# Optimization experiments

Measured on AMD Instinct MI355X. Metric: run time of the kernel, lower is better.

The kernel has to match this reference:

```python
import jax, jax.numpy as jnp
import numpy as np

D_MODEL = 1024; N_HEAD = 16; HD = 64
D_STATE = 128; D_CONV = 4; EXPAND = 2; HEADDIM = 64
D_INNER = EXPAND * D_MODEL          # 2048
NHEADS = D_INNER // HEADDIM         # 32
FFN = 4 * D_MODEL                   # 4096
B, T = 2, 1024


def rmsnorm(x, eps=1e-6):
    # FastSimpleRMSNorm: no learnable weight
    return x * jax.lax.rsqrt(jnp.mean(x * x, axis=-1, keepdims=True) + eps)


def causal_dwconv(x, w, b):
    # x: (..., T, C), w: (C, K), b: (C,). Causal depthwise conv (left pad K-1).
    K = w.shape[1]
    t = x.shape[-2]
    pad = [(0, 0)] * (x.ndim - 2) + [(K - 1, 0), (0, 0)]
    xp = jnp.pad(x, pad)
    y = jnp.zeros_like(x) + b
    for k in range(K):
        y = y + w[:, k] * jax.lax.slice_in_dim(xp, k, k + t, axis=-2)
    return y


def block_forward(x, W_in, conv_w, conv_b, A_log, Dm, dt_bias, mnorm_w, W_out,
                  W_qkv, W_cproj, qconv_w, qconv_b, kconv_w, kconv_b, vconv_w, vconv_b,
                  time_maa_k, time_maa_r, W_key, W_rec, W_val):
    Bsz, Tn, _ = x.shape
    # ---- Mamba2 branch ----
    h = rmsnorm(x)
    zxbcdt = h @ W_in                                  # (B,T,2*D_INNER+2*N+H)
    z = zxbcdt[..., :D_INNER]
    xBC = zxbcdt[..., D_INNER:2 * D_INNER + 2 * D_STATE]
    dt = zxbcdt[..., -NHEADS:]
    xBC = jax.nn.silu(causal_dwconv(xBC, conv_w, conv_b))
    xm = xBC[..., :D_INNER]
    Bm = xBC[..., D_INNER:D_INNER + D_STATE]           # (B,T,N)
    Cm = xBC[..., -D_STATE:]                           # (B,T,N)
    dt = jax.nn.softplus(dt + dt_bias)                 # (B,T,H)
    A = -jnp.exp(A_log)                                # (H,)
    xh = xm.reshape(Bsz, Tn, NHEADS, HEADDIM)          # (B,T,H,P)

    def step(hstate, inp):
        dt_t, x_t, B_t, C_t = inp                      # (B,H),(B,H,P),(B,N),(B,N)
        dA = jnp.exp(dt_t * A)                         # (B,H)
        hstate = hstate * dA[..., None, None] + (dt_t[..., None] * x_t)[..., None] * B_t[:, None, None, :]
        y_t = jnp.einsum('bhpn,bn->bhp', hstate, C_t)
        return hstate, y_t

    h0 = jnp.zeros((Bsz, NHEADS, HEADDIM, D_STATE), x.dtype)
    _, ys = jax.lax.scan(step, h0, (jnp.swapaxes(dt, 0, 1), jnp.swapaxes(xh, 0, 1),
                                    jnp.swapaxes(Bm, 0, 1), jnp.swapaxes(Cm, 0, 1)))
    y = jnp.swapaxes(ys, 0, 1) + xh * Dm[:, None]      # (B,T,H,P)
    y = y.reshape(Bsz, Tn, D_INNER) * jax.nn.silu(z)   # gated
    y = y * jax.lax.rsqrt(jnp.mean(y * y, axis=-1, keepdims=True) + 1e-5) * mnorm_w
    x = x + y @ W_out

    # ---- MQA with depthwise convs ----
    h = rmsnorm(x)
    qkv = h @ W_qkv                                    # (B,T,D_MODEL+2*HD)
    q = qkv[..., :D_MODEL].reshape(Bsz, Tn, N_HEAD, HD).transpose(0, 2, 1, 3)  # (B,H,T,D)
    k = qkv[..., D_MODEL:D_MODEL + HD]                 # (B,T,D) single kv head
    v = qkv[..., -HD:]
    q = causal_dwconv(q, qconv_w, qconv_b)
    k = causal_dwconv(k, kconv_w, kconv_b)
    v = causal_dwconv(v, vconv_w, vconv_b)
    scores = jnp.einsum('bhtd,bsd->bhts', q, k) / np.float32(np.sqrt(HD))
    mask = jnp.tril(jnp.ones((Tn, Tn), bool))
    scores = jnp.where(mask, scores, -jnp.inf)
    p = jax.nn.softmax(scores, axis=-1)
    y = jnp.einsum('bhts,bsd->bhtd', p, v)
    y = y.transpose(0, 2, 1, 3).reshape(Bsz, Tn, D_MODEL)
    x = x + y @ W_cproj

    # ---- RWKV CMix FFN ----
    h = rmsnorm(x)
    xx = jnp.pad(h, ((0, 0), (1, 0), (0, 0)))[:, :Tn] - h   # time_shift(x) - x
    xk = h + xx * time_maa_k
    xr = h + xx * time_maa_r
    kf = jnp.square(jax.nn.relu(xk @ W_key))           # ReLU^2
    kv = kf @ W_val
    x = x + jax.nn.sigmoid(xr @ W_rec) * kv
    return x


def setup_inputs() -> dict:
    key = jax.random.key(0)
    ks = jax.random.split(key, 16)
    def w(k, shape, sc=0.02):
        return jax.random.normal(k, shape, jnp.float32) * sc
    x = jax.random.normal(ks[0], (B, T, D_MODEL), jnp.float32)
    W_in = w(ks[1], (D_MODEL, 2 * D_INNER + 2 * D_STATE + NHEADS))
    conv_w = w(ks[2], (D_INNER + 2 * D_STATE, D_CONV), 0.2)
    conv_b = jnp.zeros((D_INNER + 2 * D_STATE,), jnp.float32)
    A_log = jnp.log(jnp.arange(1, NHEADS + 1, dtype=jnp.float32))
    Dm = jnp.ones((NHEADS,), jnp.float32)
    dt_bias = w(ks[3], (NHEADS,), 0.5)
    mnorm_w = jnp.ones((D_INNER,), jnp.float32)
    W_out = w(ks[4], (D_INNER, D_MODEL))
    W_qkv = w(ks[5], (D_MODEL, D_MODEL + 2 * HD))
    W_cproj = w(ks[6], (D_MODEL, D_MODEL))
    qconv_w = w(ks[7], (HD, 3), 0.3); qconv_b = jnp.zeros((HD,), jnp.float32)
    kconv_w = w(ks[8], (HD, 3), 0.3); kconv_b = jnp.zeros((HD,), jnp.float32)
    vconv_w = w(ks[9], (HD, 3), 0.3); vconv_b = jnp.zeros((HD,), jnp.float32)
    ddd = jnp.arange(D_MODEL, dtype=jnp.float32) / D_MODEL
    time_maa_k = 1.0 - ddd  # layer_id=0 -> ratio_1_to_almost0 = 1
    time_maa_r = 1.0 - ddd
    W_key = w(ks[10], (D_MODEL, FFN))
    W_rec = w(ks[11], (D_MODEL, D_MODEL))
    W_val = w(ks[12], (FFN, D_MODEL))
    return dict(x=x, W_in=W_in, conv_w=conv_w, conv_b=conv_b, A_log=A_log, Dm=Dm,
                dt_bias=dt_bias, mnorm_w=mnorm_w, W_out=W_out, W_qkv=W_qkv, W_cproj=W_cproj,
                qconv_w=qconv_w, qconv_b=qconv_b, kconv_w=kconv_w, kconv_b=kconv_b,
                vconv_w=vconv_w, vconv_b=vconv_b, time_maa_k=time_maa_k, time_maa_r=time_maa_r,
                W_key=W_key, W_rec=W_rec, W_val=W_val)


def reference(x, W_in, conv_w, conv_b, A_log, Dm, dt_bias, mnorm_w, W_out,
              W_qkv, W_cproj, qconv_w, qconv_b, kconv_w, kconv_b, vconv_w, vconv_b,
              time_maa_k, time_maa_r, W_key, W_rec, W_val):
    return block_forward(x, W_in, conv_w, conv_b, A_log, Dm, dt_bias, mnorm_w, W_out,
                         W_qkv, W_cproj, qconv_w, qconv_b, kconv_w, kconv_b, vconv_w, vconv_b,
                         time_maa_k, time_maa_r, W_key, W_rec, W_val)
```

## Files before the change

kernel.cpp:

```cpp
#include <hip/hip_runtime.h>
#include <hip/hip_bf16.h>
#include <math.h>

#define BB 2
#define TT 1024
#define BT (BB*TT)
#define DM 1024
#define DI 2048
#define DS 128
#define NHS 32
#define PDIM 64
#define NHA 16
#define HD 64
#define FFN_ 4096
#define NZX 4384
#define NXBC 2304
#define NXBCD 2336
#define CL 128
#define NC 8

typedef __hip_bfloat16 bf16;
typedef short bf16x8 __attribute__((ext_vector_type(8)));
typedef float f32x4 __attribute__((ext_vector_type(4)));

__device__ __forceinline__ float b2f(bf16 v){ return __bfloat162float(v); }
__device__ __forceinline__ bf16 f2b(float v){ return __float2bfloat16(v); }

__global__ void k_rms_in(const float* __restrict__ xin, float* __restrict__ X,
                         bf16* __restrict__ H) {
  int row = blockIdx.x;
  int tid = threadIdx.x;
  const float* xr = xin + (size_t)row * DM;
  float v[4]; float ss = 0.f;
  #pragma unroll
  for (int i = 0; i < 4; ++i) { v[i] = xr[tid*4+i]; ss += v[i]*v[i]; }
  __shared__ float red[256];
  red[tid] = ss; __syncthreads();
  for (int s = 128; s > 0; s >>= 1) { if (tid < s) red[tid] += red[tid+s]; __syncthreads(); }
  float scale = rsqrtf(red[0]/(float)DM + 1e-6f);
  float* Xr = X + (size_t)row*DM; bf16* Hr = H + (size_t)row*DM;
  #pragma unroll
  for (int i = 0; i < 4; ++i) { Xr[tid*4+i] = v[i]; Hr[tid*4+i] = f2b(v[i]*scale); }
}

__global__ void k_rms_f32(const float* __restrict__ X, bf16* __restrict__ H) {
  int row = blockIdx.x;
  int tid = threadIdx.x;
  const float* xr = X + (size_t)row * DM;
  float v[4]; float ss = 0.f;
  #pragma unroll
  for (int i = 0; i < 4; ++i) { v[i] = xr[tid*4+i]; ss += v[i]*v[i]; }
  __shared__ float red[256];
  red[tid] = ss; __syncthreads();
  for (int s = 128; s > 0; s >>= 1) { if (tid < s) red[tid] += red[tid+s]; __syncthreads(); }
  float scale = rsqrtf(red[0]/(float)DM + 1e-6f);
  bf16* Hr = H + (size_t)row*DM;
  #pragma unroll
  for (int i = 0; i < 4; ++i) Hr[tid*4+i] = f2b(v[i]*scale);
}

__global__ void k_tcast(const float* __restrict__ W, bf16* __restrict__ Wt,
                        int K, int N) {
  __shared__ float t[32][33];
  int tx = threadIdx.x, ty = threadIdx.y;
  int n0 = blockIdx.x*32, k0 = blockIdx.y*32;
  #pragma unroll
  for (int i = 0; i < 4; ++i) {
    int k = k0 + ty + i*8, n = n0 + tx;
    t[ty + i*8][tx] = (n < N) ? W[(size_t)k*N + n] : 0.f;
  }
  __syncthreads();
  #pragma unroll
  for (int i = 0; i < 4; ++i) {
    int n = n0 + ty + i*8, k = k0 + tx;
    Wt[(size_t)n*K + k] = f2b(t[tx][ty + i*8]);
  }
}

template<int EPI, bool ADD, bool OUTBF>
__global__ __launch_bounds__(256)
void mfma_gemm(const bf16* __restrict__ A, const bf16* __restrict__ Bt,
               float* __restrict__ C, bf16* __restrict__ Cbf,
               int M, int N, int K) {
  __shared__ bf16 As[128*32];
  __shared__ bf16 Bs[128*32];
  int tid = threadIdx.x;
  int wave = tid >> 6, lane = tid & 63;
  int m_l = lane & 15, quad = lane >> 4;
  int wr = (wave & 1) * 64, wc = (wave >> 1) * 64;
  int row0 = blockIdx.y * 128, col0 = blockIdx.x * 128;
  f32x4 acc[4][4];
  #pragma unroll
  for (int i = 0; i < 4; ++i)
    #pragma unroll
    for (int j = 0; j < 4; ++j) acc[i][j] = (f32x4){0.f,0.f,0.f,0.f};
  int r_a = tid >> 2;
  int kc  = (tid & 3) * 8;
  for (int k0 = 0; k0 < K; k0 += 32) {
    uint4 av0 = *(const uint4*)&A [(size_t)(row0      + r_a) * K + k0 + kc];
    uint4 av1 = *(const uint4*)&A [(size_t)(row0 + 64 + r_a) * K + k0 + kc];
    uint4 bv0 = *(const uint4*)&Bt[(size_t)(col0      + r_a) * K + k0 + kc];
    uint4 bv1 = *(const uint4*)&Bt[(size_t)(col0 + 64 + r_a) * K + k0 + kc];
    __syncthreads();
    *(uint4*)&As[(     r_a) * 32 + kc] = av0;
    *(uint4*)&As[(64 + r_a) * 32 + kc] = av1;
    *(uint4*)&Bs[(     r_a) * 32 + kc] = bv0;
    *(uint4*)&Bs[(64 + r_a) * 32 + kc] = bv1;
    __syncthreads();
    bf16x8 af[4], bfv[4];
    #pragma unroll
    for (int i = 0; i < 4; ++i) af[i]  = *(const bf16x8*)&As[(wr + i*16 + m_l)*32 + quad*8];
    #pragma unroll
    for (int j = 0; j < 4; ++j) bfv[j] = *(const bf16x8*)&Bs[(wc + j*16 + m_l)*32 + quad*8];
    #pragma unroll
    for (int i = 0; i < 4; ++i)
      #pragma unroll
      for (int j = 0; j < 4; ++j)
        acc[i][j] = __builtin_amdgcn_mfma_f32_16x16x32_bf16(af[i], bfv[j], acc[i][j], 0, 0, 0);
  }
  #pragma unroll
  for (int i = 0; i < 4; ++i) {
    #pragma unroll
    for (int j = 0; j < 4; ++j) {
      int col = col0 + wc + j*16 + m_l;
      if (col < N) {
        #pragma unroll
        for (int r = 0; r < 4; ++r) {
          int row = row0 + wr + i*16 + quad*4 + r;
          float v = acc[i][j][r];
          if (EPI == 1) { v = fmaxf(v, 0.f); v = v*v; }
          else if (EPI == 2) v = 1.f/(1.f + __expf(-v));
          if (OUTBF)      Cbf[(size_t)row*N + col] = f2b(v);
          else if (ADD)   C[(size_t)row*N + col] += v;
          else            C[(size_t)row*N + col]  = v;
        }
      }
    }
  }
}

__global__ __launch_bounds__(256)
void mfma_sk32(const bf16* __restrict__ A, const bf16* __restrict__ Bt,
               float* __restrict__ P0, float* __restrict__ P1,
               float* __restrict__ P2, float* __restrict__ P3,
               int M, int N, int K, int kchunk) {
  __shared__ bf16 As[128*32];
  __shared__ bf16 Bs[128*32];
  int tid = threadIdx.x;
  int wave = tid >> 6, lane = tid & 63;
  int m_l = lane & 15, quad = lane >> 4;
  int wr = (wave & 1) * 64, wc = (wave >> 1) * 64;
  int row0 = blockIdx.y * 128, col0 = blockIdx.x * 128;
  int kbeg = blockIdx.z * kchunk;
  int kend = kbeg + kchunk;
  f32x4 acc[4][4];
  #pragma unroll
  for (int i = 0; i < 4; ++i)
    #pragma unroll
    for (int j = 0; j < 4; ++j) acc[i][j] = (f32x4){0.f,0.f,0.f,0.f};
  int r_a = tid >> 2;
  int kc  = (tid & 3) * 8;
  for (int k0 = kbeg; k0 < kend; k0 += 32) {
    uint4 av0 = *(const uint4*)&A [(size_t)(row0      + r_a) * K + k0 + kc];
    uint4 av1 = *(const uint4*)&A [(size_t)(row0 + 64 + r_a) * K + k0 + kc];
    uint4 bv0 = *(const uint4*)&Bt[(size_t)(col0      + r_a) * K + k0 + kc];
    uint4 bv1 = *(const uint4*)&Bt[(size_t)(col0 + 64 + r_a) * K + k0 + kc];
    __syncthreads();
    *(uint4*)&As[(     r_a) * 32 + kc] = av0;
    *(uint4*)&As[(64 + r_a) * 32 + kc] = av1;
    *(uint4*)&Bs[(     r_a) * 32 + kc] = bv0;
    *(uint4*)&Bs[(64 + r_a) * 32 + kc] = bv1;
    __syncthreads();
    bf16x8 af[4], bfv[4];
    #pragma unroll
    for (int i = 0; i < 4; ++i) af[i]  = *(const bf16x8*)&As[(wr + i*16 + m_l)*32 + quad*8];
    #pragma unroll
    for (int j = 0; j < 4; ++j) bfv[j] = *(const bf16x8*)&Bs[(wc + j*16 + m_l)*32 + quad*8];
    #pragma unroll
    for (int i = 0; i < 4; ++i)
      #pragma unroll
      for (int j = 0; j < 4; ++j)
        acc[i][j] = __builtin_amdgcn_mfma_f32_16x16x32_bf16(af[i], bfv[j], acc[i][j], 0, 0, 0);
  }
  float* P = (blockIdx.z == 0) ? P0 : (blockIdx.z == 1) ? P1 : (blockIdx.z == 2) ? P2 : P3;
  #pragma unroll
  for (int i = 0; i < 4; ++i) {
    #pragma unroll
    for (int j = 0; j < 4; ++j) {
      int col = col0 + wc + j*16 + m_l;
      if (col < N) {
        #pragma unroll
        for (int r = 0; r < 4; ++r) {
          int row = row0 + wr + i*16 + quad*4 + r;
          P[(size_t)row*N + col] = acc[i][j][r];
        }
      }
    }
  }
}

template<int Z, int EPI, bool ADD>
__global__ void k_reduce(float* __restrict__ dst, const float* __restrict__ p0,
                         const float* __restrict__ p1, const float* __restrict__ p2,
                         const float* __restrict__ p3) {
  size_t i = ((size_t)blockIdx.x*256 + threadIdx.x)*4;
  float4 a = *(const float4*)(p0 + i);
  float4 b = *(const float4*)(p1 + i);
  float r0 = a.x + b.x, r1 = a.y + b.y, r2 = a.z + b.z, r3 = a.w + b.w;
  if (Z == 4) {
    float4 c = *(const float4*)(p2 + i);
    float4 d = *(const float4*)(p3 + i);
    r0 += c.x + d.x; r1 += c.y + d.y; r2 += c.z + d.z; r3 += c.w + d.w;
  }
  if (EPI == 2) {
    r0 = 1.f/(1.f + __expf(-r0)); r1 = 1.f/(1.f + __expf(-r1));
    r2 = 1.f/(1.f + __expf(-r2)); r3 = 1.f/(1.f + __expf(-r3));
  }
  if (ADD) {
    float4 o = *(const float4*)(dst + i);
    r0 += o.x; r1 += o.y; r2 += o.z; r3 += o.w;
  }
  float4 res; res.x = r0; res.y = r1; res.z = r2; res.w = r3;
  *(float4*)(dst + i) = res;
}

__global__ void k_conv_ssm(const float* __restrict__ ZXr, const float* __restrict__ cw,
                           const float* __restrict__ cb, const float* __restrict__ dtb,
                           bf16* __restrict__ XBCb, float* __restrict__ DT) {
  int bt = blockIdx.x; int b = bt >> 10; int t = bt & 1023;
  int tid = threadIdx.x;
  for (int c = tid; c < NXBC; c += 256) {
    float acc = cb[c];
    #pragma unroll
    for (int kk = 0; kk < 4; ++kk) {
      int ts = t - 3 + kk;
      if (ts >= 0) acc += cw[c*4+kk] * ZXr[((size_t)(b*TT+ts))*NXBCD + c];
    }
    float s = acc / (1.f + __expf(-acc));
    XBCb[(size_t)bt*NXBC + c] = f2b(s);
  }
  if (tid < NHS) {
    float x = ZXr[(size_t)bt*NXBCD + NXBC + tid] + dtb[tid];
    float sp = (x > 20.f) ? x : log1pf(__expf(x));
    DT[(size_t)bt*NHS + tid] = sp;
  }
}

__global__ __launch_bounds__(256)
void k_scan1(const bf16* __restrict__ xbcb, const float* __restrict__ dt,
             const float* __restrict__ A_log, const float* __restrict__ Dmv,
             float* __restrict__ Y, float* __restrict__ SC, float* __restrict__ CUM) {
  int bc = blockIdx.x;
  int bh = bc >> 3, c = bc & 7;
  int b = bh >> 5, h = bh & 31;
  int tid = threadIdx.x, wave = tid >> 6, lane = tid & 63;
  int col = lane & 15, quad = lane >> 4;
  int t0 = c * CL;
  __shared__ bf16 sB[128*136];
  __shared__ bf16 sC[128*136];
  __shared__ bf16 sxT[64*136];
  __shared__ float sL[128], sdt[128];
  float A = -__expf(A_log[h]);
  float Dmh = Dmv[h];
  for (int e = tid; e < 128*16; e += 256) {
    int r = e >> 4, ch = e & 15;
    const bf16* row = xbcb + (size_t)(b*TT + t0 + r)*NXBC;
    *(uint4*)&sB[r*136 + ch*8] = *(const uint4*)&row[2048 + ch*8];
    *(uint4*)&sC[r*136 + ch*8] = *(const uint4*)&row[2176 + ch*8];
  }
  for (int e = tid; e < 64*128; e += 256) {
    int p = e & 63, t = e >> 6;
    sxT[p*136 + t] = xbcb[(size_t)(b*TT + t0 + t)*NXBC + h*64 + p];
  }
  if (tid < 128) sdt[tid] = dt[(size_t)(b*TT + t0 + tid)*NHS + h];
  __syncthreads();
  if (wave == 0) {
    float a0 = sdt[2*lane]*A, a1 = sdt[2*lane+1]*A;
    float tot = a0 + a1;
    #pragma unroll
    for (int off = 1; off < 64; off <<= 1) {
      float up = __shfl_up(tot, off);
      if (lane >= off) tot += up;
    }
    sL[2*lane+1] = tot;
    sL[2*lane]   = tot - a1;
  }
  __syncthreads();
  int wr = (wave & 1)*64, wc = (wave >> 1)*64;
  f32x4 g[4][4];
  #pragma unroll
  for (int i = 0; i < 4; ++i)
    #pragma unroll
    for (int j = 0; j < 4; ++j) g[i][j] = (f32x4){0.f,0.f,0.f,0.f};
  #pragma unroll
  for (int kf = 0; kf < 4; ++kf) {
    bf16x8 af[4], bfr[4];
    #pragma unroll
    for (int i = 0; i < 4; ++i) af[i]  = *(const bf16x8*)&sC[(wr + i*16 + col)*136 + kf*32 + quad*8];
    #pragma unroll
    for (int j = 0; j < 4; ++j) bfr[j] = *(const bf16x8*)&sB[(wc + j*16 + col)*136 + kf*32 + quad*8];
    #pragma unroll
    for (int i = 0; i < 4; ++i)
      #pragma unroll
      for (int j = 0; j < 4; ++j)
        g[i][j] = __builtin_amdgcn_mfma_f32_16x16x32_bf16(af[i], bfr[j], g[i][j], 0, 0, 0);
  }
  __syncthreads();
  if (tid < 128) CUM[(size_t)bh*TT + t0 + tid] = __expf(sL[tid]);
  float Lend = sL[127];
  #pragma unroll
  for (int i = 0; i < 4; ++i) {
    #pragma unroll
    for (int j = 0; j < 4; ++j) {
      int sl = wc + j*16 + col;
      #pragma unroll
      for (int r = 0; r < 4; ++r) {
        int tl = wr + i*16 + quad*4 + r;
        float v = (sl <= tl) ? g[i][j][r] * __expf(sL[tl] - sL[sl]) * sdt[sl] : 0.f;
        sC[tl*136 + sl] = f2b(v);
      }
    }
  }
  for (int e = tid; e < 128*128; e += 256) {
    int n = e & 127, s = e >> 7;
    float w = __expf(Lend - sL[s]) * sdt[s];
    sB[n*136 + s] = f2b(b2f(xbcb[(size_t)(b*TT + t0 + s)*NXBC + 2048 + n]) * w);
  }
  __syncthreads();
  f32x4 ya[2][4];
  #pragma unroll
  for (int i2 = 0; i2 < 2; ++i2)
    #pragma unroll
    for (int jd = 0; jd < 4; ++jd) ya[i2][jd] = (f32x4){0.f,0.f,0.f,0.f};
  #pragma unroll
  for (int kf = 0; kf < 4; ++kf) {
    bf16x8 pa[2], xa[4];
    #pragma unroll
    for (int i2 = 0; i2 < 2; ++i2)
      pa[i2] = *(const bf16x8*)&sC[(wave*32 + i2*16 + col)*136 + kf*32 + quad*8];
    #pragma unroll
    for (int jd = 0; jd < 4; ++jd)
      xa[jd] = *(const bf16x8*)&sxT[(jd*16 + col)*136 + kf*32 + quad*8];
    #pragma unroll
    for (int i2 = 0; i2 < 2; ++i2)
      #pragma unroll
      for (int jd = 0; jd < 4; ++jd)
        ya[i2][jd] = __builtin_amdgcn_mfma_f32_16x16x32_bf16(pa[i2], xa[jd], ya[i2][jd], 0, 0, 0);
  }
  #pragma unroll
  for (int i2 = 0; i2 < 2; ++i2) {
    #pragma unroll
    for (int jd = 0; jd < 4; ++jd) {
      int p = jd*16 + col;
      #pragma unroll
      for (int r = 0; r < 4; ++r) {
        int tl = wave*32 + i2*16 + quad*4 + r;
        float xv = b2f(sxT[p*136 + tl]);
        Y[(size_t)(b*TT + t0 + tl)*DI + h*64 + p] = ya[i2][jd][r] + xv*Dmh;
      }
    }
  }
  f32x4 sa[8];
  #pragma unroll
  for (int nt = 0; nt < 8; ++nt) sa[nt] = (f32x4){0.f,0.f,0.f,0.f};
  #pragma unroll
  for (int kf = 0; kf < 4; ++kf) {
    bf16x8 xpa = *(const bf16x8*)&sxT[(wave*16 + col)*136 + kf*32 + quad*8];
    #pragma unroll
    for (int nt = 0; nt < 8; ++nt) {
      bf16x8 bwa = *(const bf16x8*)&sB[(nt*16 + col)*136 + kf*32 + quad*8];
      sa[nt] = __builtin_amdgcn_mfma_f32_16x16x32_bf16(xpa, bwa, sa[nt], 0, 0, 0);
    }
  }
  #pragma unroll
  for (int nt = 0; nt < 8; ++nt) {
    int n = nt*16 + col;
    #pragma unroll
    for (int r = 0; r < 4; ++r) {
      int p = wave*16 + quad*4 + r;
      SC[((size_t)(bh*NC + c)*64 + p)*128 + n] = sa[nt][r];
    }
  }
}

__global__ __launch_bounds__(512)
void k_scan2(float* __restrict__ SC, const float* __restrict__ CUM) {
  int bh = blockIdx.x;
  int tid = threadIdx.x;
  int p = tid >> 3, g = tid & 7;
  float S[16];
  #pragma unroll
  for (int j = 0; j < 16; ++j) S[j] = 0.f;
  for (int c = 0; c < NC; ++c) {
    size_t base = ((size_t)(bh*NC + c)*64 + p)*128 + g*16;
    float Ptot = CUM[(size_t)bh*TT + c*CL + (CL-1)];
    float tmp[16];
    #pragma unroll
    for (int j = 0; j < 16; ++j) tmp[j] = SC[base + j];
    #pragma unroll
    for (int j = 0; j < 16; ++j) SC[base + j] = S[j];
    #pragma unroll
    for (int j = 0; j < 16; ++j) S[j] = S[j]*Ptot + tmp[j];
  }
}

__global__ __launch_bounds__(256)
void k_scan3(const bf16* __restrict__ xbcb, const float* __restrict__ SC,
             const float* __restrict__ CUM, float* __restrict__ Y) {
  int bc = blockIdx.x;
  int bh = bc >> 3, c = bc & 7;
  if (c == 0) return;
  int b = bh >> 5, h = bh & 31;
  int tid = threadIdx.x, wave = tid >> 6, lane = tid & 63;
  int col = lane & 15, quad = lane >> 4;
  int t0 = c * CL;
  __shared__ bf16 sCt[128*136];
  __shared__ bf16 sS[64*136];
  __shared__ float sCum[128];
  for (int e = tid; e < 128*16; e += 256) {
    int r = e >> 4, ch = e & 15;
    *(uint4*)&sCt[r*136 + ch*8] =
      *(const uint4*)&xbcb[(size_t)(b*TT + t0 + r)*NXBC + 2176 + ch*8];
  }
  for (int e = tid; e < 64*128; e += 256) {
    int n = e & 127, p = e >> 7;
    sS[p*136 + n] = f2b(SC[((size_t)(bh*NC + c)*64 + p)*128 + n]);
  }
  if (tid < 128) sCum[tid] = CUM[(size_t)bh*TT + t0 + tid];
  __syncthreads();
  f32x4 ya[2][4];
  #pragma unroll
  for (int i2 = 0; i2 < 2; ++i2)
    #pragma unroll
    for (int jd = 0; jd < 4; ++jd) ya[i2][jd] = (f32x4){0.f,0.f,0.f,0.f};
  #pragma unroll
  for (int kf = 0; kf < 4; ++kf) {
    bf16x8 pa[2], sv[4];
    #pragma unroll
    for (int i2 = 0; i2 < 2; ++i2)
      pa[i2] = *(const bf16x8*)&sCt[(wave*32 + i2*16 + col)*136 + kf*32 + quad*8];
    #pragma unroll
    for (int jd = 0; jd < 4; ++jd)
      sv[jd] = *(const bf16x8*)&sS[(jd*16 + col)*136 + kf*32 + quad*8];
    #pragma unroll
    for (int i2 = 0; i2 < 2; ++i2)
      #pragma unroll
      for (int jd = 0; jd < 4; ++jd)
        ya[i2][jd] = __builtin_amdgcn_mfma_f32_16x16x32_bf16(pa[i2], sv[jd], ya[i2][jd], 0, 0, 0);
  }
  #pragma unroll
  for (int i2 = 0; i2 < 2; ++i2) {
    #pragma unroll
    for (int jd = 0; jd < 4; ++jd) {
      int p = jd*16 + col;
      #pragma unroll
      for (int r = 0; r < 4; ++r) {
        int tl = wave*32 + i2*16 + quad*4 + r;
        Y[(size_t)(b*TT + t0 + tl)*DI + h*64 + p] += sCum[tl]*ya[i2][jd][r];
      }
    }
  }
}

__global__ void k_gate(const float* __restrict__ Y, const float* __restrict__ Z,
                       const float* __restrict__ mnw, bf16* __restrict__ Ybf) {
  int row = blockIdx.x; int tid = threadIdx.x;
  const float* yr = Y + (size_t)row*DI;
  const float* zr = Z + (size_t)row*DI;
  float gv[8]; float ss = 0.f;
  #pragma unroll
  for (int i = 0; i < 8; ++i) {
    int c = tid*8 + i;
    float z = zr[c];
    float sz = z / (1.f + __expf(-z));
    float v = yr[c]*sz;
    gv[i] = v; ss += v*v;
  }
  __shared__ float red[256];
  red[tid] = ss; __syncthreads();
  for (int s = 128; s > 0; s >>= 1) { if (tid < s) red[tid] += red[tid+s]; __syncthreads(); }
  float scale = rsqrtf(red[0]/(float)DI + 1e-5f);
  bf16* br = Ybf + (size_t)row*DI;
  #pragma unroll
  for (int i = 0; i < 8; ++i) { int c = tid*8 + i; br[c] = f2b(gv[i]*scale*mnw[c]); }
}

__global__ void k_conv_qkv(const float* __restrict__ QKV,
                           const float* qw, const float* qb, const float* kw, const float* kb,
                           const float* vw, const float* vb,
                           bf16* __restrict__ Qb, bf16* __restrict__ Kb, bf16* __restrict__ Vtb) {
  int bt = blockIdx.x; int b = bt >> 10; int t = bt & 1023;
  int tid = threadIdx.x;
  for (int c = tid; c < 1152; c += 256) {
    if (c < 1024) {
      int h = c >> 6, d = c & 63;
      float acc = qb[d];
      #pragma unroll
      for (int kk = 0; kk < 3; ++kk) { int ts = t-2+kk; if (ts >= 0) acc += qw[d*3+kk] * QKV[((size_t)(b*TT+ts))*1152 + c]; }
      Qb[((size_t)(b*NHA + h)*TT + t)*HD + d] = f2b(acc * 0.125f);
    } else if (c < 1088) {
      int d = c - 1024;
      float acc = kb[d];
      #pragma unroll
      for (int kk = 0; kk < 3; ++kk) { int ts = t-2+kk; if (ts >= 0) acc += kw[d*3+kk] * QKV[((size_t)(b*TT+ts))*1152 + c]; }
      Kb[(size_t)bt*HD + d] = f2b(acc);
    } else {
      int d = c - 1088;
      float acc = vb[d];
      #pragma unroll
      for (int kk = 0; kk < 3; ++kk) { int ts = t-2+kk; if (ts >= 0) acc += vw[d*3+kk] * QKV[((size_t)(b*TT+ts))*1152 + c]; }
      Vtb[((size_t)(b*HD + d))*TT + t] = f2b(acc);
    }
  }
}

__global__ __launch_bounds__(256)
void k_flash(const bf16* __restrict__ Qb, const bf16* __restrict__ Kb,
             const bf16* __restrict__ Vtb, bf16* __restrict__ out) {
  int qt = blockIdx.x, h = blockIdx.y, b = blockIdx.z;
  int tid = threadIdx.x, wave = tid >> 6, lane = tid & 63;
  int col = lane & 15, quad = lane >> 4;
  int t0 = qt * 128;
  __shared__ bf16 Ks[128*72];
  __shared__ bf16 Vs[64*136];
  __shared__ bf16 Ps[4][32*136];
  const bf16* Qbase = Qb + ((size_t)(b*NHA + h))*TT*HD;
  bf16x8 qf[2][2];
  #pragma unroll
  for (int i = 0; i < 2; ++i)
    #pragma unroll
    for (int kf = 0; kf < 2; ++kf)
      qf[i][kf] = *(const bf16x8*)&Qbase[(size_t)(t0 + wave*32 + i*16 + col)*HD + kf*32 + quad*8];
  float mst[2][4], lst[2][4];
  f32x4 oacc[2][4];
  #pragma unroll
  for (int i = 0; i < 2; ++i)
    #pragma unroll
    for (int r = 0; r < 4; ++r) { mst[i][r] = -1e30f; lst[i][r] = 0.f; }
  #pragma unroll
  for (int i = 0; i < 2; ++i)
    #pragma unroll
    for (int jd = 0; jd < 4; ++jd) oacc[i][jd] = (f32x4){0.f,0.f,0.f,0.f};

  for (int kt = 0; kt <= qt; ++kt) {
    int s0 = kt * 128;
    __syncthreads();
    for (int e = tid; e < 1024; e += 256) {
      int r = e >> 3, ch = e & 7;
      *(uint4*)&Ks[r*72 + ch*8] = *(const uint4*)&Kb[((size_t)(b*TT + s0 + r))*HD + ch*8];
    }
    for (int e = tid; e < 1024; e += 256) {
      int d = e >> 4, ch = e & 15;
      *(uint4*)&Vs[d*136 + ch*8] = *(const uint4*)&Vtb[((size_t)(b*HD + d))*TT + s0 + ch*8];
    }
    __syncthreads();
    f32x4 sacc[2][8];
    #pragma unroll
    for (int i = 0; i < 2; ++i)
      #pragma unroll
      for (int j = 0; j < 8; ++j) sacc[i][j] = (f32x4){0.f,0.f,0.f,0.f};
    #pragma unroll
    for (int j = 0; j < 8; ++j) {
      bf16x8 kf0 = *(const bf16x8*)&Ks[(j*16 + col)*72 + quad*8];
      bf16x8 kf1 = *(const bf16x8*)&Ks[(j*16 + col)*72 + 32 + quad*8];
      #pragma unroll
      for (int i = 0; i < 2; ++i) {
        sacc[i][j] = __builtin_amdgcn_mfma_f32_16x16x32_bf16(qf[i][0], kf0, sacc[i][j], 0, 0, 0);
        sacc[i][j] = __builtin_amdgcn_mfma_f32_16x16x32_bf16(qf[i][1], kf1, sacc[i][j], 0, 0, 0);
      }
    }
    bool diag = (kt == qt);
    #pragma unroll
    for (int i = 0; i < 2; ++i) {
      #pragma unroll
      for (int r = 0; r < 4; ++r) {
        int rowloc = wave*32 + i*16 + quad*4 + r;
        if (diag) {
          #pragma unroll
          for (int j = 0; j < 8; ++j)
            if (j*16 + col > rowloc) sacc[i][j][r] = -1e30f;
        }
        float mx = -1e30f;
        #pragma unroll
        for (int j = 0; j < 8; ++j) mx = fmaxf(mx, sacc[i][j][r]);
        mx = fmaxf(mx, __shfl_xor(mx, 1));
        mx = fmaxf(mx, __shfl_xor(mx, 2));
        mx = fmaxf(mx, __shfl_xor(mx, 4));
        mx = fmaxf(mx, __shfl_xor(mx, 8));
        float nm = fmaxf(mst[i][r], mx);
        float alpha = __expf(mst[i][r] - nm);
        float sum = 0.f;
        #pragma unroll
        for (int j = 0; j < 8; ++j) {
          float pv = __expf(sacc[i][j][r] - nm);
          sacc[i][j][r] = pv; sum += pv;
        }
        sum += __shfl_xor(sum, 1);
        sum += __shfl_xor(sum, 2);
        sum += __shfl_xor(sum, 4);
        sum += __shfl_xor(sum, 8);
        lst[i][r] = lst[i][r]*alpha + sum;
        mst[i][r] = nm;
        #pragma unroll
        for (int jd = 0; jd < 4; ++jd) oacc[i][jd][r] *= alpha;
      }
    }
    #pragma unroll
    for (int i = 0; i < 2; ++i)
      #pragma unroll
      for (int j = 0; j < 8; ++j)
        #pragma unroll
        for (int r = 0; r < 4; ++r)
          Ps[wave][(i*16 + quad*4 + r)*136 + j*16 + col] = f2b(sacc[i][j][r]);
    #pragma unroll
    for (int i = 0; i < 2; ++i) {
      bf16x8 pa[4];
      #pragma unroll
      for (int kf = 0; kf < 4; ++kf)
        pa[kf] = *(const bf16x8*)&Ps[wave][(i*16 + col)*136 + kf*32 + quad*8];
      #pragma unroll
      for (int jd = 0; jd < 4; ++jd) {
        #pragma unroll
        for (int kf = 0; kf < 4; ++kf) {
          bf16x8 vbf = *(const bf16x8*)&Vs[(jd*16 + col)*136 + kf*32 + quad*8];
          oacc[i][jd] = __builtin_amdgcn_mfma_f32_16x16x32_bf16(pa[kf], vbf, oacc[i][jd], 0, 0, 0);
        }
      }
    }
  }
  #pragma unroll
  for (int i = 0; i < 2; ++i) {
    #pragma unroll
    for (int jd = 0; jd < 4; ++jd) {
      int d = jd*16 + col;
      #pragma unroll
      for (int r = 0; r < 4; ++r) {
        int t = t0 + wave*32 + i*16 + quad*4 + r;
        out[((size_t)(b*TT + t))*DM + h*64 + d] = f2b(oacc[i][jd][r] / lst[i][r]);
      }
    }
  }
}

__global__ void k_tshift(const bf16* __restrict__ H, const float* __restrict__ maak,
                         const float* __restrict__ maar,
                         bf16* __restrict__ XK, bf16* __restrict__ XR) {
  int idx = blockIdx.x*256 + threadIdx.x;
  int c = idx & (DM - 1);
  int bt = idx >> 10;
  int t = bt & (TT - 1);
  float h = b2f(H[idx]);
  float prev = (t > 0) ? b2f(H[idx - DM]) : 0.f;
  float xx = prev - h;
  XK[idx] = f2b(h + xx*maak[c]);
  XR[idx] = f2b(h + xx*maar[c]);
}

__global__ void k_final(const float* __restrict__ X, const float* __restrict__ R,
                        const float* __restrict__ KV, float* __restrict__ out) {
  int idx = blockIdx.x*256 + threadIdx.x;
  out[idx] = X[idx] + R[idx]*KV[idx];
}

extern "C" void kernel_launch(void* const* d_in, const int* in_sizes, int n_in,
                              void* d_out, int out_size, void* d_ws, size_t ws_size,
                              hipStream_t stream) {
  const float* x_in    = (const float*)d_in[0];
  const float* W_in    = (const float*)d_in[1];
  const float* conv_w  = (const float*)d_in[2];
  const float* conv_b  = (const float*)d_in[3];
  const float* A_log   = (const float*)d_in[4];
  const float* Dm      = (const float*)d_in[5];
  const float* dt_bias = (const float*)d_in[6];
  const float* mnorm_w = (const float*)d_in[7];
  const float* W_out   = (const float*)d_in[8];
  const float* W_qkv   = (const float*)d_in[9];
  const float* W_cproj = (const float*)d_in[10];
  const float* qconv_w = (const float*)d_in[11];
  const float* qconv_b = (const float*)d_in[12];
  const float* kconv_w = (const float*)d_in[13];
  const float* kconv_b = (const float*)d_in[14];
  const float* vconv_w = (const float*)d_in[15];
  const float* vconv_b = (const float*)d_in[16];
  const float* maa_k   = (const float*)d_in[17];
  const float* maa_r   = (const float*)d_in[18];
  const float* W_key   = (const float*)d_in[19];
  const float* W_rec   = (const float*)d_in[20];
  const float* W_val   = (const float*)d_in[21];
  float* out = (float*)d_out;

  float* ws = (float*)d_ws;
  float* X       = ws;
  bf16*  Hbf     = (bf16*)(ws + 2097152);
  float* Zbuf    = ws + 3145728;
  float* XBCDraw = ws + 7340032;
  float* XBC     = ws + 12124160;
  float* DT      = ws + 16842752;
  float* CUM     = ws + 16908288;
  float* Y       = ws + 16973824;

  bf16*  Wt_in    = (bf16*)XBC;
  bf16*  XBCb     = (bf16*)XBC;
  float* SC       = XBCDraw;
  bf16*  Ybf      = (bf16*)XBC;
  bf16*  Wt_out   = (bf16*)(XBC + 2097152);
  float* QKV      = Zbuf;
  bf16*  Wt_qkv   = (bf16*)XBC;
  bf16*  Qb       = (bf16*)XBCDraw;
  bf16*  Kb       = (bf16*)(XBCDraw + 1048576);
  bf16*  Vtb      = (bf16*)(XBCDraw + 1114112);
  bf16*  ATTNbf   = (bf16*)Y;
  bf16*  Wt_cproj = (bf16*)(Y + 1048576);
  bf16*  XKbf     = (bf16*)XBC;
  bf16*  XRbf     = (bf16*)(XBC + 1048576);
  bf16*  Wt_key   = (bf16*)Zbuf;
  bf16*  KFbf     = (bf16*)XBCDraw;
  bf16*  Wt_val   = (bf16*)Zbuf;
  float* KV       = Y;
  float* R        = Y + 2097152;
  bf16*  Wt_rec   = (bf16*)Zbuf;

  dim3 thr256(256), thr512(512);
  dim3 tblk(32, 8);

  k_rms_in<<<BT, thr256, 0, stream>>>(x_in, X, Hbf);
  k_tcast<<<dim3(4480/32, 1024/32), tblk, 0, stream>>>(W_in, Wt_in, 1024, NZX);
  mfma_gemm<0,false,false><<<dim3(16, 16), thr256, 0, stream>>>(Hbf, Wt_in, Zbuf, nullptr, BT, 2048, 1024);
  mfma_gemm<0,false,false><<<dim3(19, 16), thr256, 0, stream>>>(Hbf, Wt_in + (size_t)2048*1024, XBCDraw, nullptr, BT, NXBCD, 1024);
  k_conv_ssm<<<BT, thr256, 0, stream>>>(XBCDraw, conv_w, conv_b, dt_bias, XBCb, DT);
  k_scan1<<<BB*NHS*NC, thr256, 0, stream>>>(XBCb, DT, A_log, Dm, Y, SC, CUM);
  k_scan2<<<BB*NHS, thr512, 0, stream>>>(SC, CUM);
  k_scan3<<<BB*NHS*NC, thr256, 0, stream>>>(XBCb, SC, CUM, Y);
  k_gate<<<BT, thr256, 0, stream>>>(Y, Zbuf, mnorm_w, Ybf);
  k_tcast<<<dim3(1024/32, 2048/32), tblk, 0, stream>>>(W_out, Wt_out, 2048, 1024);
  mfma_sk32<<<dim3(8, 16, 4), thr256, 0, stream>>>(Ybf, Wt_out,
      Zbuf, Zbuf + 2097152, XBCDraw, XBCDraw + 2097152, BT, 1024, 2048, 512);
  k_reduce<4,0,true><<<2048, thr256, 0, stream>>>(X, Zbuf, Zbuf + 2097152, XBCDraw, XBCDraw + 2097152);
  k_rms_f32<<<BT, thr256, 0, stream>>>(X, Hbf);
  k_tcast<<<dim3(1152/32, 1024/32), tblk, 0, stream>>>(W_qkv, Wt_qkv, 1024, 1152);
  mfma_sk32<<<dim3(9, 16, 2), thr256, 0, stream>>>(Hbf, Wt_qkv,
      XBCDraw, XBCDraw + 2359296, XBCDraw, XBCDraw, BT, 1152, 1024, 512);
  k_reduce<2,0,false><<<2304, thr256, 0, stream>>>(QKV, XBCDraw, XBCDraw + 2359296, XBCDraw, XBCDraw);
  k_conv_qkv<<<BT, thr256, 0, stream>>>(QKV, qconv_w, qconv_b, kconv_w, kconv_b, vconv_w, vconv_b, Qb, Kb, Vtb);
  k_flash<<<dim3(TT/128, NHA, BB), thr256, 0, stream>>>(Qb, Kb, Vtb, ATTNbf);
  k_tcast<<<dim3(1024/32, 1024/32), tblk, 0, stream>>>(W_cproj, Wt_cproj, 1024, 1024);
  mfma_sk32<<<dim3(8, 16, 2), thr256, 0, stream>>>(ATTNbf, Wt_cproj,
      XBC, XBC + 2097152, XBC, XBC, BT, 1024, 1024, 512);
  k_reduce<2,0,true><<<2048, thr256, 0, stream>>>(X, XBC, XBC + 2097152, XBC, XBC);
  k_rms_f32<<<BT, thr256, 0, stream>>>(X, Hbf);
  k_tshift<<<(BT*DM)/256, thr256, 0, stream>>>(Hbf, maa_k, maa_r, XKbf, XRbf);
  k_tcast<<<dim3(4096/32, 1024/32), tblk, 0, stream>>>(W_key, Wt_key, 1024, 4096);
  mfma_gemm<1,false,true><<<dim3(32, 16), thr256, 0, stream>>>(XKbf, Wt_key, nullptr, KFbf, BT, 4096, 1024);
  k_tcast<<<dim3(1024/32, 4096/32), tblk, 0, stream>>>(W_val, Wt_val, 4096, 1024);
  mfma_sk32<<<dim3(8, 16, 4), thr256, 0, stream>>>(KFbf, Wt_val,
      Y, Y + 2097152, XBC + 2621440, Zbuf + 2097152, BT, 1024, 4096, 1024);
  k_reduce<4,0,false><<<2048, thr256, 0, stream>>>(KV, Y, Y + 2097152, XBC + 2621440, Zbuf + 2097152);
  k_tcast<<<dim3(1024/32, 1024/32), tblk, 0, stream>>>(W_rec, Wt_rec, 1024, 1024);
  mfma_sk32<<<dim3(8, 16, 2), thr256, 0, stream>>>(XRbf, Wt_rec,
      Y + 2097152, XBC + 2621440, Y, Y, BT, 1024, 1024, 512);
  k_reduce<2,2,false><<<2048, thr256, 0, stream>>>(R, Y + 2097152, XBC + 2621440, Y, Y);
  k_final<<<(BT*DM)/256, thr256, 0, stream>>>(X, R, KV, out);
}
```

Baseline: 593.0 us.

## Split flash attention KV range across two blocks and combine partials

Flash attention now splits each query tile's causal KV range into two halves handled by separate blocks. Each block writes unnormalized fp32 partial outputs plus running max and sum, and a new combine kernel merges them with log-sum-exp weighting. The K and V shared-memory staging and its barriers are removed, so MFMA operands are loaded straight from global memory. This is meant to balance the causal workload and raise occupancy on a small grid, at the cost of extra fp32 partial traffic, one more launch, and uncoalesced global operand loads.

After: 598.4 us. Within noise of the previous version (+0.9%).

```diff
diff --git a/kernel.cpp b/kernel.cpp
--- a/kernel.cpp
+++ b/kernel.cpp
@@ -515,16 +515,23 @@
 }
 
 __global__ __launch_bounds__(256)
-void k_flash(const bf16* __restrict__ Qb, const bf16* __restrict__ Kb,
-             const bf16* __restrict__ Vtb, bf16* __restrict__ out) {
-  int qt = blockIdx.x, h = blockIdx.y, b = blockIdx.z;
+void k_flash_sk(const bf16* __restrict__ Qb, const bf16* __restrict__ Kb,
+                const bf16* __restrict__ Vtb, float* __restrict__ Op,
+                float* __restrict__ Mp, float* __restrict__ Lp) {
+  int qt = blockIdx.x >> 1, z = blockIdx.x & 1;
+  int h = blockIdx.y, b = blockIdx.z;
+  int n = qt + 1;
+  int kmid = (n + 1) >> 1;
+  int kbeg = z ? kmid : 0;
+  int kend = z ? n : kmid;
+  if (kbeg >= kend) return;
   int tid = threadIdx.x, wave = tid >> 6, lane = tid & 63;
   int col = lane & 15, quad = lane >> 4;
   int t0 = qt * 128;
-  __shared__ bf16 Ks[128*72];
-  __shared__ bf16 Vs[64*136];
   __shared__ bf16 Ps[4][32*136];
   const bf16* Qbase = Qb + ((size_t)(b*NHA + h))*TT*HD;
+  const bf16* Kbase = Kb + (size_t)b*TT*HD;
+  const bf16* Vbase = Vtb + (size_t)b*HD*TT;
   bf16x8 qf[2][2];
   #pragma unroll
   for (int i = 0; i < 2; ++i)
@@ -542,18 +549,8 @@
     #pragma unroll
     for (int jd = 0; jd < 4; ++jd) oacc[i][jd] = (f32x4){0.f,0.f,0.f,0.f};
 
-  for (int kt = 0; kt <= qt; ++kt) {
+  for (int kt = kbeg; kt < kend; ++kt) {
     int s0 = kt * 128;
-    __syncthreads();
-    for (int e = tid; e < 1024; e += 256) {
-      int r = e >> 3, ch = e & 7;
-      *(uint4*)&Ks[r*72 + ch*8] = *(const uint4*)&Kb[((size_t)(b*TT + s0 + r))*HD + ch*8];
-    }
-    for (int e = tid; e < 1024; e += 256) {
-      int d = e >> 4, ch = e & 15;
-      *(uint4*)&Vs[d*136 + ch*8] = *(const uint4*)&Vtb[((size_t)(b*HD + d))*TT + s0 + ch*8];
-    }
-    __syncthreads();
     f32x4 sacc[2][8];
     #pragma unroll
     for (int i = 0; i < 2; ++i)
@@ -561,8 +558,8 @@
       for (int j = 0; j < 8; ++j) sacc[i][j] = (f32x4){0.f,0.f,0.f,0.f};
     #pragma unroll
     for (int j = 0; j < 8; ++j) {
-      bf16x8 kf0 = *(const bf16x8*)&Ks[(j*16 + col)*72 + quad*8];
-      bf16x8 kf1 = *(const bf16x8*)&Ks[(j*16 + col)*72 + 32 + quad*8];
+      bf16x8 kf0 = *(const bf16x8*)&Kbase[(size_t)(s0 + j*16 + col)*HD + quad*8];
+      bf16x8 kf1 = *(const bf16x8*)&Kbase[(size_t)(s0 + j*16 + col)*HD + 32 + quad*8];
       #pragma unroll
       for (int i = 0; i < 2; ++i) {
         sacc[i][j] = __builtin_amdgcn_mfma_f32_16x16x32_bf16(qf[i][0], kf0, sacc[i][j], 0, 0, 0);
@@ -622,12 +619,13 @@
       for (int jd = 0; jd < 4; ++jd) {
         #pragma unroll
         for (int kf = 0; kf < 4; ++kf) {
-          bf16x8 vbf = *(const bf16x8*)&Vs[(jd*16 + col)*136 + kf*32 + quad*8];
+          bf16x8 vbf = *(const bf16x8*)&Vbase[(size_t)(jd*16 + col)*TT + s0 + kf*32 + quad*8];
           oacc[i][jd] = __builtin_amdgcn_mfma_f32_16x16x32_bf16(pa[kf], vbf, oacc[i][jd], 0, 0, 0);
         }
       }
     }
   }
+  size_t robase = ((size_t)((z*BB + b)*NHA + h))*TT + t0;
   #pragma unroll
   for (int i = 0; i < 2; ++i) {
     #pragma unroll
@@ -635,11 +633,49 @@
       int d = jd*16 + col;
       #pragma unroll
       for (int r = 0; r < 4; ++r) {
-        int t = t0 + wave*32 + i*16 + quad*4 + r;
-        out[((size_t)(b*TT + t))*DM + h*64 + d] = f2b(oacc[i][jd][r] / lst[i][r]);
-      }
-    }
-  }
+        int tl = wave*32 + i*16 + quad*4 + r;
+        Op[(robase + tl)*HD + d] = oacc[i][jd][r];
+      }
+    }
+  }
+  if (col == 0) {
+    #pragma unroll
+    for (int i = 0; i < 2; ++i)
+      #pragma unroll
+      for (int r = 0; r < 4; ++r) {
+        int tl = wave*32 + i*16 + quad*4 + r;
+        Mp[robase + tl] = mst[i][r];
+        Lp[robase + tl] = lst[i][r];
+      }
+  }
+}
+
+__global__ void k_att_comb(const float* __restrict__ Op, const float* __restrict__ Mp,
+                           const float* __restrict__ Lp, bf16* __restrict__ outb) {
+  int idx = blockIdx.x*256 + threadIdx.x;
+  int e = idx*4;
+  int c = e & (DM - 1); int h = c >> 6; int d = c & 63;
+  int bt = e >> 10; int t = bt & (TT - 1); int b = bt >> 10;
+  int qt = t >> 7;
+  size_t r0 = ((size_t)(b*NHA + h))*TT + t;
+  float4 o0 = *(const float4*)&Op[r0*HD + d];
+  float m0 = Mp[r0], l0 = Lp[r0];
+  float ox, oy, oz, ow;
+  if (qt > 0) {
+    size_t r1 = ((size_t)((BB + b)*NHA + h))*TT + t;
+    float4 o1 = *(const float4*)&Op[r1*HD + d];
+    float m1 = Mp[r1], l1 = Lp[r1];
+    float M = fmaxf(m0, m1);
+    float w0 = __expf(m0 - M), w1 = __expf(m1 - M);
+    float inv = 1.f / (w0*l0 + w1*l1);
+    ox = (w0*o0.x + w1*o1.x)*inv; oy = (w0*o0.y + w1*o1.y)*inv;
+    oz = (w0*o0.z + w1*o1.z)*inv; ow = (w0*o0.w + w1*o1.w)*inv;
+  } else {
+    float inv = 1.f / l0;
+    ox = o0.x*inv; oy = o0.y*inv; oz = o0.z*inv; ow = o0.w*inv;
+  }
+  bf16* p = outb + (size_t)bt*DM + c;
+  p[0] = f2b(ox); p[1] = f2b(oy); p[2] = f2b(oz); p[3] = f2b(ow);
 }
 
 __global__ void k_tshift(const bf16* __restrict__ H, const float* __restrict__ maak,
@@ -719,6 +755,9 @@
   float* KV       = Y;
   float* R        = Y + 2097152;
   bf16*  Wt_rec   = (bf16*)Zbuf;
+  float* FOp      = Zbuf;
+  float* FMp      = ws + 2097152;
+  float* FLp      = ws + 2162688;
 
   dim3 thr256(256), thr512(512);
   dim3 tblk(32, 8);
@@ -742,7 +781,8 @@
       XBCDraw, XBCDraw + 2359296, XBCDraw, XBCDraw, BT, 1152, 1024, 512);
   k_reduce<2,0,false><<<2304, thr256, 0, stream>>>(QKV, XBCDraw, XBCDraw + 2359296, XBCDraw, XBCDraw);
   k_conv_qkv<<<BT, thr256, 0, stream>>>(QKV, qconv_w, qconv_b, kconv_w, kconv_b, vconv_w, vconv_b, Qb, Kb, Vtb);
-  k_flash<<<dim3(TT/128, NHA, BB), thr256, 0, stream>>>(Qb, Kb, Vtb, ATTNbf);
+  k_flash_sk<<<dim3((TT/128)*2, NHA, BB), thr256, 0, stream>>>(Qb, Kb, Vtb, FOp, FMp, FLp);
+  k_att_comb<<<(BT*DM)/(256*4), thr256, 0, stream>>>(FOp, FMp, FLp, ATTNbf);
   k_tcast<<<dim3(1024/32, 1024/32), tblk, 0, stream>>>(W_cproj, Wt_cproj, 1024, 1024);
   mfma_sk32<<<dim3(8, 16, 2), thr256, 0, stream>>>(ATTNbf, Wt_cproj,
       XBC, XBC + 2097152, XBC, XBC, BT, 1024, 1024, 512);
```
